# Kernel tuning notes

Hardware: AMD Instinct MI355X
Metric: run time of the kernel (lower is better)

## Reference

```python
import jax, jax.numpy as jnp
import numpy as np


def setup_inputs() -> dict:
    key = jax.random.key(0)
    ks = jax.random.split(key, 6)
    B, T, D, U = 32, 2048, 512, 512
    scale = 1.0 / np.sqrt(D)
    return {
        "values": jax.random.normal(ks[0], (B, T, D), dtype=jnp.float32),
        "query": jax.random.normal(ks[1], (B, D), dtype=jnp.float32),
        "W1": jax.random.normal(ks[2], (D, U), dtype=jnp.float32) * scale,
        "b1": jnp.zeros((U,), dtype=jnp.float32),
        "W2": jax.random.normal(ks[3], (D, U), dtype=jnp.float32) * scale,
        "b2": jnp.zeros((U,), dtype=jnp.float32),
        "V": jax.random.normal(ks[4], (U, 1), dtype=jnp.float32) * (1.0 / np.sqrt(U)),
        "bV": jnp.zeros((1,), dtype=jnp.float32),
    }


def reference(values, query, W1, b1, W2, b2, V, bV):
    # values: [B,T,D], query: [B,D]
    proj_v = jnp.einsum("btd,du->btu", values, W1) + b1          # [B,T,U]
    proj_q = (query @ W2 + b2)[:, None, :]                        # [B,1,U]
    score = jnp.tanh(proj_v + proj_q) @ V + bV                    # [B,T,1]
    attention_weights = jax.nn.softmax(score, axis=1)             # [B,T,1]
    context_vector = jnp.sum(attention_weights * values, axis=1)  # [B,D]
    return context_vector, attention_weights
```

## Files before the change

### kernel.cpp

```cpp
#include <hip/hip_runtime.h>
#include <math.h>


#define B_ 32
#define T_ 2048
#define D_ 512
#define U_ 512
#define M_ (B_ * T_)

typedef _Float16 half8 __attribute__((ext_vector_type(8)));
typedef float floatx4 __attribute__((ext_vector_type(4)));

__global__ __launch_bounds__(256) void projq_kernel(
    const float* __restrict__ query, const float* __restrict__ W2,
    const float* __restrict__ b2, float* __restrict__ projq) {
  const int b = blockIdx.x;
  const int u = blockIdx.y * 256 + threadIdx.x;
  __shared__ float q[D_];
  for (int d = threadIdx.x; d < D_; d += 256) q[d] = query[b * D_ + d];
  __syncthreads();
  float acc = 0.f;
#pragma unroll 8
  for (int d = 0; d < D_; ++d) acc += q[d] * W2[d * U_ + u];
  projq[b * U_ + u] = acc + b2[u];
}

__global__ __launch_bounds__(256) void score_mfma_kernel(
    const float* __restrict__ values, const float* __restrict__ W1,
    const float* __restrict__ b1, const float* __restrict__ projq,
    const float* __restrict__ V, float* __restrict__ scores) {
  const int m0 = blockIdx.x * 128;
  const int u0 = blockIdx.y * 128;
  const int b = blockIdx.x >> 4;
  const int tid = threadIdx.x;

  __shared__ alignas(16) _Float16 As[128 * 32];
  __shared__ alignas(16) _Float16 Bs[128 * 32];

  const int lane = tid & 63;
  const int w = tid >> 6;
  const int wm = (w & 1) * 64;
  const int wn = (w >> 1) * 64;
  const int ln = lane & 15;
  const int lq = lane >> 4;

  floatx4 acc[4][4] = {};

  const int srow = tid >> 1;
  const int skoff = (tid & 1) * 16;
  const float* aptr = values + (long)(m0 + srow) * D_ + skoff;
  const float* bptr = W1 + u0 + srow;

  for (int k0 = 0; k0 < D_; k0 += 32) {
    const float4 a0 = *(const float4*)(aptr + k0);
    const float4 a1 = *(const float4*)(aptr + k0 + 4);
    const float4 a2 = *(const float4*)(aptr + k0 + 8);
    const float4 a3 = *(const float4*)(aptr + k0 + 12);
    half8 ha0 = {(_Float16)a0.x, (_Float16)a0.y, (_Float16)a0.z, (_Float16)a0.w,
                 (_Float16)a1.x, (_Float16)a1.y, (_Float16)a1.z, (_Float16)a1.w};
    half8 ha1 = {(_Float16)a2.x, (_Float16)a2.y, (_Float16)a2.z, (_Float16)a2.w,
                 (_Float16)a3.x, (_Float16)a3.y, (_Float16)a3.z, (_Float16)a3.w};
    float bt[16];
#pragma unroll
    for (int kk = 0; kk < 16; ++kk)
      bt[kk] = bptr[(long)(k0 + skoff + kk) * U_];
    half8 hb0 = {(_Float16)bt[0], (_Float16)bt[1], (_Float16)bt[2], (_Float16)bt[3],
                 (_Float16)bt[4], (_Float16)bt[5], (_Float16)bt[6], (_Float16)bt[7]};
    half8 hb1 = {(_Float16)bt[8], (_Float16)bt[9], (_Float16)bt[10], (_Float16)bt[11],
                 (_Float16)bt[12], (_Float16)bt[13], (_Float16)bt[14], (_Float16)bt[15]};

    *(half8*)&As[srow * 32 + skoff] = ha0;
    *(half8*)&As[srow * 32 + skoff + 8] = ha1;
    *(half8*)&Bs[srow * 32 + skoff] = hb0;
    *(half8*)&Bs[srow * 32 + skoff + 8] = hb1;
    __syncthreads();

    half8 af[4], bf[4];
#pragma unroll
    for (int i = 0; i < 4; ++i) {
      af[i] = *(const half8*)&As[(wm + i * 16 + ln) * 32 + lq * 8];
      bf[i] = *(const half8*)&Bs[(wn + i * 16 + ln) * 32 + lq * 8];
    }
#pragma unroll
    for (int mi = 0; mi < 4; ++mi)
#pragma unroll
      for (int ni = 0; ni < 4; ++ni)
        acc[mi][ni] = __builtin_amdgcn_mfma_f32_16x16x32_f16(
            af[mi], bf[ni], acc[mi][ni], 0, 0, 0);
    __syncthreads();
  }

  float pre[4], vv[4];
#pragma unroll
  for (int ni = 0; ni < 4; ++ni) {
    const int u = u0 + wn + ni * 16 + ln;
    pre[ni] = b1[u] + projq[b * U_ + u];
    vv[ni] = V[u];
  }
#pragma unroll
  for (int mi = 0; mi < 4; ++mi) {
#pragma unroll
    for (int r = 0; r < 4; ++r) {
      float t = 0.f;
#pragma unroll
      for (int ni = 0; ni < 4; ++ni)
        t += tanhf(acc[mi][ni][r] + pre[ni]) * vv[ni];
      t += __shfl_xor(t, 1);
      t += __shfl_xor(t, 2);
      t += __shfl_xor(t, 4);
      t += __shfl_xor(t, 8);
      if (ln == mi * 4 + r)
        atomicAdd(scores + m0 + wm + mi * 16 + lq * 4 + r, t);
    }
  }
}

__global__ __launch_bounds__(256) void softmax_kernel(
    const float* __restrict__ scores, float* __restrict__ weights) {
  const int b = blockIdx.x;
  const int tid = threadIdx.x;
  float v[8];
  float mx = -INFINITY;
#pragma unroll
  for (int i = 0; i < 8; ++i) {
    v[i] = scores[b * T_ + i * 256 + tid];
    mx = fmaxf(mx, v[i]);
  }
#pragma unroll
  for (int off = 32; off > 0; off >>= 1) mx = fmaxf(mx, __shfl_down(mx, off));
  __shared__ float sm[4], ss[4];
  if ((tid & 63) == 0) sm[tid >> 6] = mx;
  __syncthreads();
  mx = fmaxf(fmaxf(sm[0], sm[1]), fmaxf(sm[2], sm[3]));
  float sum = 0.f;
#pragma unroll
  for (int i = 0; i < 8; ++i) {
    v[i] = __expf(v[i] - mx);
    sum += v[i];
  }
#pragma unroll
  for (int off = 32; off > 0; off >>= 1) sum += __shfl_down(sum, off);
  if ((tid & 63) == 0) ss[tid >> 6] = sum;
  __syncthreads();
  const float inv = 1.f / (ss[0] + ss[1] + ss[2] + ss[3]);
#pragma unroll
  for (int i = 0; i < 8; ++i) weights[b * T_ + i * 256 + tid] = v[i] * inv;
}

__global__ __launch_bounds__(256) void context_kernel(
    const float* __restrict__ values, const float* __restrict__ weights,
    float* __restrict__ context) {
  const int b = blockIdx.x;
  const int t0 = blockIdx.y * 64;
  const int tid = threadIdx.x;
  __shared__ float w[64];
  if (tid < 64) w[tid] = weights[b * T_ + t0 + tid];
  __syncthreads();
  float2 acc = make_float2(0.f, 0.f);
  const float2* vp = (const float2*)(values + (long)(b * T_ + t0) * D_) + tid;
#pragma unroll 4
  for (int t = 0; t < 64; ++t) {
    const float2 x = vp[(long)t * (D_ / 2)];
    acc.x += w[t] * x.x;
    acc.y += w[t] * x.y;
  }
  atomicAdd(context + b * D_ + tid * 2 + 0, acc.x);
  atomicAdd(context + b * D_ + tid * 2 + 1, acc.y);
}

extern "C" void kernel_launch(void* const* d_in, const int* in_sizes, int n_in,
                              void* d_out, int out_size, void* d_ws, size_t ws_size,
                              hipStream_t stream) {
  const float* values = (const float*)d_in[0];
  const float* query = (const float*)d_in[1];
  const float* W1 = (const float*)d_in[2];
  const float* b1 = (const float*)d_in[3];
  const float* W2 = (const float*)d_in[4];
  const float* b2 = (const float*)d_in[5];
  const float* V = (const float*)d_in[6];

  float* out = (float*)d_out;
  float* context = out;
  float* weights = out + B_ * D_;
  float* projq = (float*)d_ws;
  float* scores = projq + B_ * U_;

  hipMemsetAsync(scores, 0, M_ * sizeof(float), stream);
  hipMemsetAsync(context, 0, B_ * D_ * sizeof(float), stream);

  projq_kernel<<<dim3(B_, U_ / 256), 256, 0, stream>>>(query, W2, b2, projq);
  score_mfma_kernel<<<dim3(M_ / 128, U_ / 128), 256, 0, stream>>>(
      values, W1, b1, projq, V, scores);
  softmax_kernel<<<B_, 256, 0, stream>>>(scores, weights);
  context_kernel<<<dim3(B_, T_ / 64), 256, 0, stream>>>(values, weights, context);
}
```

Before: 361.0 us.

## Pre-transpose W1 to fp16 and load MFMA fragments directly from global memory

Adds a prep kernel that transposes W1 into an fp16 [U,D] buffer in workspace. The score kernel then loads A and B fragments straight from global memory into registers, with no LDS staging or barriers. This removes the strided per-element W1 loads, the repeated fp16 conversion and the syncthreads. tanhf is also replaced by an exp-based fast tanh. The trade-offs are uncoalesced-ish fragment loads from global memory, reliance on L2 for reuse, and a workspace-size gate that falls back to the old path.

After: 409.1 us. 13.3% more time.

```diff
diff --git a/kernel.cpp b/kernel.cpp
--- a/kernel.cpp
+++ b/kernel.cpp
@@ -10,6 +10,12 @@
 
 typedef _Float16 half8 __attribute__((ext_vector_type(8)));
 typedef float floatx4 __attribute__((ext_vector_type(4)));
+
+__device__ __forceinline__ float fast_tanh(float x) {
+  x = fminf(fmaxf(x, -20.f), 20.f);
+  const float e = __expf(2.f * x);
+  return 1.f - 2.f / (e + 1.f);
+}
 
 __global__ __launch_bounds__(256) void projq_kernel(
     const float* __restrict__ query, const float* __restrict__ W2,
@@ -25,6 +31,92 @@
   projq[b * U_ + u] = acc + b2[u];
 }
 
+__global__ __launch_bounds__(256) void prep_w1t(
+    const float* __restrict__ W1, _Float16* __restrict__ w1t) {
+  __shared__ float t[64][65];
+  const int k0 = blockIdx.x * 64, u0 = blockIdx.y * 64;
+  const int lu = threadIdx.x & 63;
+  const int g = threadIdx.x >> 6;
+#pragma unroll
+  for (int i = 0; i < 16; ++i) {
+    const int row = g * 16 + i;
+    t[row][lu] = W1[(long)(k0 + row) * U_ + u0 + lu];
+  }
+  __syncthreads();
+#pragma unroll
+  for (int i = 0; i < 16; ++i) {
+    const int row = g * 16 + i;
+    w1t[(long)(u0 + row) * D_ + k0 + lu] = (_Float16)t[lu][row];
+  }
+}
+
+__global__ __launch_bounds__(256) void score_direct_kernel(
+    const float* __restrict__ values, const _Float16* __restrict__ w1t,
+    const float* __restrict__ b1, const float* __restrict__ projq,
+    const float* __restrict__ V, float* __restrict__ scores) {
+  const int m0 = blockIdx.x * 128;
+  const int u0 = blockIdx.y * 128;
+  const int b = blockIdx.x >> 4;
+  const int tid = threadIdx.x;
+  const int lane = tid & 63;
+  const int w = tid >> 6;
+  const int wm = (w & 1) * 64;
+  const int wn = (w >> 1) * 64;
+  const int ln = lane & 15;
+  const int lq = lane >> 4;
+
+  const float* aBase = values + (long)(m0 + wm + ln) * D_ + lq * 8;
+  const _Float16* bBase = w1t + (long)(u0 + wn + ln) * D_ + lq * 8;
+
+  floatx4 acc[4][4] = {};
+
+  for (int k0 = 0; k0 < D_; k0 += 32) {
+    half8 af[4];
+#pragma unroll
+    for (int mi = 0; mi < 4; ++mi) {
+      const float* p = aBase + (long)mi * 16 * D_ + k0;
+      const float4 x = *(const float4*)p;
+      const float4 y = *(const float4*)(p + 4);
+      af[mi] = half8{(_Float16)x.x, (_Float16)x.y, (_Float16)x.z, (_Float16)x.w,
+                     (_Float16)y.x, (_Float16)y.y, (_Float16)y.z, (_Float16)y.w};
+    }
+    half8 bf[4];
+#pragma unroll
+    for (int ni = 0; ni < 4; ++ni)
+      bf[ni] = *(const half8*)(bBase + (long)ni * 16 * D_ + k0);
+#pragma unroll
+    for (int mi = 0; mi < 4; ++mi)
+#pragma unroll
+      for (int ni = 0; ni < 4; ++ni)
+        acc[mi][ni] = __builtin_amdgcn_mfma_f32_16x16x32_f16(
+            af[mi], bf[ni], acc[mi][ni], 0, 0, 0);
+  }
+
+  float pre[4], vv[4];
+#pragma unroll
+  for (int ni = 0; ni < 4; ++ni) {
+    const int u = u0 + wn + ni * 16 + ln;
+    pre[ni] = b1[u] + projq[b * U_ + u];
+    vv[ni] = V[u];
+  }
+#pragma unroll
+  for (int mi = 0; mi < 4; ++mi) {
+#pragma unroll
+    for (int r = 0; r < 4; ++r) {
+      float t = 0.f;
+#pragma unroll
+      for (int ni = 0; ni < 4; ++ni)
+        t += fast_tanh(acc[mi][ni][r] + pre[ni]) * vv[ni];
+      t += __shfl_xor(t, 1);
+      t += __shfl_xor(t, 2);
+      t += __shfl_xor(t, 4);
+      t += __shfl_xor(t, 8);
+      if (ln == mi * 4 + r)
+        atomicAdd(scores + m0 + wm + mi * 16 + lq * 4 + r, t);
+    }
+  }
+}
+
 __global__ __launch_bounds__(256) void score_mfma_kernel(
     const float* __restrict__ values, const float* __restrict__ W1,
     const float* __restrict__ b1, const float* __restrict__ projq,
@@ -33,24 +125,19 @@
   const int u0 = blockIdx.y * 128;
   const int b = blockIdx.x >> 4;
   const int tid = threadIdx.x;
-
   __shared__ alignas(16) _Float16 As[128 * 32];
   __shared__ alignas(16) _Float16 Bs[128 * 32];
-
   const int lane = tid & 63;
   const int w = tid >> 6;
   const int wm = (w & 1) * 64;
   const int wn = (w >> 1) * 64;
   const int ln = lane & 15;
   const int lq = lane >> 4;
-
   floatx4 acc[4][4] = {};
-
   const int srow = tid >> 1;
   const int skoff = (tid & 1) * 16;
   const float* aptr = values + (long)(m0 + srow) * D_ + skoff;
   const float* bptr = W1 + u0 + srow;
-
   for (int k0 = 0; k0 < D_; k0 += 32) {
     const float4 a0 = *(const float4*)(aptr + k0);
     const float4 a1 = *(const float4*)(aptr + k0 + 4);
@@ -68,13 +155,11 @@
                  (_Float16)bt[4], (_Float16)bt[5], (_Float16)bt[6], (_Float16)bt[7]};
     half8 hb1 = {(_Float16)bt[8], (_Float16)bt[9], (_Float16)bt[10], (_Float16)bt[11],
                  (_Float16)bt[12], (_Float16)bt[13], (_Float16)bt[14], (_Float16)bt[15]};
-
     *(half8*)&As[srow * 32 + skoff] = ha0;
     *(half8*)&As[srow * 32 + skoff + 8] = ha1;
     *(half8*)&Bs[srow * 32 + skoff] = hb0;
     *(half8*)&Bs[srow * 32 + skoff + 8] = hb1;
     __syncthreads();
-
     half8 af[4], bf[4];
 #pragma unroll
     for (int i = 0; i < 4; ++i) {
@@ -89,7 +174,6 @@
             af[mi], bf[ni], acc[mi][ni], 0, 0, 0);
     __syncthreads();
   }
-
   float pre[4], vv[4];
 #pragma unroll
   for (int ni = 0; ni < 4; ++ni) {
@@ -104,7 +188,7 @@
       float t = 0.f;
 #pragma unroll
       for (int ni = 0; ni < 4; ++ni)
-        t += tanhf(acc[mi][ni][r] + pre[ni]) * vv[ni];
+        t += fast_tanh(acc[mi][ni][r] + pre[ni]) * vv[ni];
       t += __shfl_xor(t, 1);
       t += __shfl_xor(t, 2);
       t += __shfl_xor(t, 4);
@@ -184,13 +268,22 @@
   float* weights = out + B_ * D_;
   float* projq = (float*)d_ws;
   float* scores = projq + B_ * U_;
+  _Float16* w1t = (_Float16*)((char*)d_ws + 65536 + 262144);
+
+  const bool fast = ws_size >= (size_t)(65536 + 262144 + 524288);
 
   hipMemsetAsync(scores, 0, M_ * sizeof(float), stream);
   hipMemsetAsync(context, 0, B_ * D_ * sizeof(float), stream);
 
   projq_kernel<<<dim3(B_, U_ / 256), 256, 0, stream>>>(query, W2, b2, projq);
-  score_mfma_kernel<<<dim3(M_ / 128, U_ / 128), 256, 0, stream>>>(
-      values, W1, b1, projq, V, scores);
+  if (fast) {
+    prep_w1t<<<dim3(D_ / 64, U_ / 64), 256, 0, stream>>>(W1, w1t);
+    score_direct_kernel<<<dim3(M_ / 128, U_ / 128), 256, 0, stream>>>(
+        values, w1t, b1, projq, V, scores);
+  } else {
+    score_mfma_kernel<<<dim3(M_ / 128, U_ / 128), 256, 0, stream>>>(
+        values, W1, b1, projq, V, scores);
+  }
   softmax_kernel<<<B_, 256, 0, stream>>>(scores, weights);
   context_kernel<<<dim3(B_, T_ / 64), 256, 0, stream>>>(values, weights, context);
 }
```
